# Optimization experiments

Measured on AMD Instinct MI355X. Metric: run time of the kernel, lower is better.

The kernel has to match this reference:

```python
import jax, jax.numpy as jnp
import numpy as np

B, H, S, D = 2, 16, 2048, 64  # batch, heads, seq (q_len=k_len), head dim (d_k=d_v)


def setup_inputs() -> dict:
    key = jax.random.key(0)
    kq, kk, kv = jax.random.split(key, 3)
    Q = jax.random.normal(kq, (B, H, S, D), dtype=jnp.float32)
    K = jax.random.normal(kk, (B, H, S, D), dtype=jnp.float32)
    V = jax.random.normal(kv, (B, H, S, D), dtype=jnp.float32)
    # causal 0/1 mask [q_len, k_len]; zeros get filled with -inf like masked_fill_
    mask = jnp.tril(jnp.ones((S, S), dtype=jnp.int32))
    return {"Q": Q, "K": K, "V": V, "mask": mask}


def reference(Q, K, V, mask):
    scale = K.shape[-1] ** 0.5
    # [B,H,q,k] = Q @ K^T / sqrt(d_k)
    scores = jnp.einsum("bhqd,bhkd->bhqk", Q, K) / scale
    # mask broadcast over batch/heads; mask==0 -> -inf
    scores = jnp.where(mask == 0, jnp.float32(-jnp.inf), scores)
    attn = jax.nn.softmax(scores, axis=-1)
    return jnp.einsum("bhqk,bhkd->bhqd", attn, V)
```

## Files before the change

kernel.cpp:

```cpp
#include <hip/hip_runtime.h>

#define S_LEN 2048
#define DHEAD 64
#define BK 64
#define NBH 32
#define QSCALE 0.18033688011112042f
#define THR 8.0f

typedef float f32x4 __attribute__((ext_vector_type(4)));
typedef __bf16 bf16x8 __attribute__((ext_vector_type(8)));
typedef unsigned short u16x8 __attribute__((ext_vector_type(8)));
typedef unsigned short u16x4 __attribute__((ext_vector_type(4)));
typedef unsigned int   u32x4 __attribute__((ext_vector_type(4)));
typedef unsigned int   u32x2 __attribute__((ext_vector_type(2)));

static __device__ __forceinline__ unsigned short bfr(float f) {
    return __builtin_bit_cast(unsigned short, (__bf16)f);
}
static __device__ __forceinline__ int swz(int row, int cb) {
    return row * 128 + (cb ^ ((row & 7) << 4));
}

#if __has_builtin(__builtin_amdgcn_permlane32_swap) && __has_builtin(__builtin_amdgcn_permlane16_swap)
#define HAVE_PLSWAP 1
static __device__ __forceinline__ void plswap32(unsigned& a, unsigned& b) {
    u32x2 r = __builtin_amdgcn_permlane32_swap(a, b, false, false);
    a = r[0]; b = r[1];
}
static __device__ __forceinline__ void plswap16(unsigned& a, unsigned& b) {
    u32x2 r = __builtin_amdgcn_permlane16_swap(a, b, false, false);
    a = r[0]; b = r[1];
}
static __device__ __forceinline__ float bcast_max4(float x) {
    unsigned a = __builtin_bit_cast(unsigned, x), b = a;
    plswap16(a, b);
    float m = fmaxf(__builtin_bit_cast(float, a), __builtin_bit_cast(float, b));
    unsigned c = __builtin_bit_cast(unsigned, m), d = c;
    plswap32(c, d);
    return fmaxf(__builtin_bit_cast(float, c), __builtin_bit_cast(float, d));
}
static __device__ __forceinline__ float bcast_sum4(float x) {
    unsigned a = __builtin_bit_cast(unsigned, x), b = a;
    plswap16(a, b);
    float s = __builtin_bit_cast(float, a) + __builtin_bit_cast(float, b);
    unsigned c = __builtin_bit_cast(unsigned, s), d = c;
    plswap32(c, d);
    return __builtin_bit_cast(float, c) + __builtin_bit_cast(float, d);
}
#else
#define HAVE_PLSWAP 0
static __device__ __forceinline__ void plswap32(unsigned& a, unsigned& b) {
    asm("v_permlane32_swap_b32 %0, %1" : "+v"(a), "+v"(b));
}
static __device__ __forceinline__ void plswap16(unsigned& a, unsigned& b) {
    asm("v_permlane16_swap_b32 %0, %1" : "+v"(a), "+v"(b));
}
static __device__ __forceinline__ float bcast_max4(float x) {
    x = fmaxf(x, __shfl_xor(x, 16));
    return fmaxf(x, __shfl_xor(x, 32));
}
static __device__ __forceinline__ float bcast_sum4(float x) {
    x += __shfl_xor(x, 16);
    return x + __shfl_xor(x, 32);
}
#endif

__global__ __launch_bounds__(256)
void cvt_bf16(const float* __restrict__ src, unsigned short* __restrict__ dst, int n4) {
    const int stride = gridDim.x * blockDim.x;
    for (int i = blockIdx.x * blockDim.x + threadIdx.x; i < n4; i += stride) {
        f32x4 v = ((const f32x4*)src)[i];
        u16x4 t;
        t[0] = bfr(v[0]); t[1] = bfr(v[1]); t[2] = bfr(v[2]); t[3] = bfr(v[3]);
        ((u16x4*)dst)[i] = t;
    }
}

__global__ __launch_bounds__(256)
void cvt_transpose_v(const float* __restrict__ V, unsigned short* __restrict__ Vt) {
    __shared__ unsigned short t2[64][72];
    const int bh = (int)blockIdx.x >> 5;
    const int st = (int)blockIdx.x & 31;
    const int t  = threadIdx.x;
    {
        const int sl = t >> 2, d0 = (t & 3) * 16;
        const float* src = V + ((size_t)bh * S_LEN + st * 64 + sl) * DHEAD + d0;
#pragma unroll
        for (int j = 0; j < 4; ++j) {
            f32x4 v = *(const f32x4*)(src + j * 4);
#pragma unroll
            for (int e = 0; e < 4; ++e) t2[sl][d0 + j * 4 + e] = bfr(v[e]);
        }
    }
    __syncthreads();
    const int d = t >> 2, sc = (t & 3) * 16;
    u16x8 a, b;
#pragma unroll
    for (int r = 0; r < 8; ++r) { a[r] = t2[sc + r][d]; b[r] = t2[sc + 8 + r][d]; }
    unsigned short* dst = Vt + ((size_t)bh * DHEAD + d) * S_LEN + st * 64 + sc;
    *(u16x8*)dst = a;
    *(u16x8*)(dst + 8) = b;
}

__global__ __launch_bounds__(256, 4)
void attn16r(const float* __restrict__ Qg,
             const unsigned short* __restrict__ Kb,
             const unsigned short* __restrict__ Vt,
             float* __restrict__ Og) {
    __shared__ __align__(16) unsigned short sK[2][BK * DHEAD];
    __shared__ __align__(16) unsigned short sV[2][DHEAD * BK];

    const int tid  = threadIdx.x;
    const int lane = tid & 63;
    const int w    = tid >> 6;
    const int idx = (int)blockIdx.x >> 5;
    const int bh  = (int)blockIdx.x & (NBH - 1);
    const int jj  = idx & 7, k4 = idx >> 3;
    const int blk_q = (k4 == 0) ? 31 - jj : (k4 == 1) ? jj
                    : (k4 == 2) ? 16 + jj : 15 - jj;
    const int q0 = blk_q * 64;
    const size_t base = (size_t)bh * (S_LEN * DHEAD);

    const int c = lane & 15;
    const int h = lane >> 4;

    const int srow = w * 8 + (lane >> 3);
    const int ch8  = ((lane & 7) ^ (lane >> 3)) * 8;
    const unsigned short* pK = Kb + base + (size_t)srow * DHEAD + ch8;
    const unsigned short* pV = Vt + base + (size_t)srow * S_LEN + ch8;

    auto issue = [&](int buf, int kt) {
        unsigned short* dK = &sK[buf][w * 512];
        unsigned short* dV = &sV[buf][w * 512];
        const unsigned short* gk = pK + (size_t)kt * 4096;
        const unsigned short* gv = pV + kt * 64;
#pragma unroll
        for (int i = 0; i < 2; ++i) {
            __builtin_amdgcn_global_load_lds(
                (const __attribute__((address_space(1))) unsigned int*)(gk + i * 2048),
                (__attribute__((address_space(3))) unsigned int*)(dK + i * 2048),
                16, 0, 0);
            __builtin_amdgcn_global_load_lds(
                (const __attribute__((address_space(1))) unsigned int*)(gv + (size_t)i * 32 * S_LEN),
                (__attribute__((address_space(3))) unsigned int*)(dV + i * 2048),
                16, 0, 0);
        }
    };

    bf16x8 qf[2];
    {
        const int qrow = q0 + w * 16 + c;
        const float* qp = Qg + base + (size_t)qrow * DHEAD + h * 8;
#pragma unroll
        for (int kk = 0; kk < 2; ++kk) {
            f32x4 a = *(const f32x4*)(qp + kk * 32);
            f32x4 b = *(const f32x4*)(qp + kk * 32 + 4);
            u16x8 t;
#pragma unroll
            for (int j = 0; j < 4; ++j) {
                t[j]     = bfr(a[j] * QSCALE);
                t[4 + j] = bfr(b[j] * QSCALE);
            }
            qf[kk] = __builtin_bit_cast(bf16x8, t);
        }
    }

    int offAB[4][2];
#pragma unroll
    for (int n = 0; n < 4; ++n)
#pragma unroll
        for (int kk = 0; kk < 2; ++kk)
            offAB[n][kk] = swz(n * 16 + c, (kk * 32 + h * 8) * 2);

    f32x4 o[4];
#pragma unroll
    for (int dn = 0; dn < 4; ++dn) o[dn] = (f32x4){0.f, 0.f, 0.f, 0.f};
    float m_run = -INFINITY, l_run = 0.f;

    issue(0, 0);
    int cur = 0;
    for (int kt = 0; kt <= blk_q; ++kt) {
        __syncthreads();
        if (kt < blk_q) issue(cur ^ 1, kt + 1);

        const char* sKc = (const char*)&sK[cur][0];
        const char* sVc = (const char*)&sV[cur][0];

        f32x4 st[4];
#pragma unroll
        for (int n = 0; n < 4; ++n) {
            f32x4 acc = (f32x4){0.f, 0.f, 0.f, 0.f};
#pragma unroll
            for (int kk = 0; kk < 2; ++kk) {
                u16x8 kf = *(const u16x8*)(sKc + offAB[n][kk]);
                acc = __builtin_amdgcn_mfma_f32_16x16x32_bf16(
                        __builtin_bit_cast(bf16x8, kf), qf[kk], acc, 0, 0, 0);
            }
            st[n] = acc;
        }

        bf16x8 vf[4][2];
#pragma unroll
        for (int dn = 0; dn < 4; ++dn)
#pragma unroll
            for (int kk = 0; kk < 2; ++kk)
                vf[dn][kk] = __builtin_bit_cast(bf16x8,
                                *(const u16x8*)(sVc + offAB[dn][kk]));

        if (kt == blk_q) {
            const int qg = q0 + w * 16 + c;
#pragma unroll
            for (int n = 0; n < 4; ++n)
#pragma unroll
                for (int r = 0; r < 4; ++r)
                    if (kt * BK + n * 16 + 4 * h + r > qg) st[n][r] = -INFINITY;
        }

        float mx = fmaxf(fmaxf(st[0][0], st[0][1]), fmaxf(st[0][2], st[0][3]));
#pragma unroll
        for (int n = 1; n < 4; ++n)
            mx = fmaxf(mx, fmaxf(fmaxf(st[n][0], st[n][1]), fmaxf(st[n][2], st[n][3])));
        mx = bcast_max4(mx);
        if (__any(mx > m_run + THR)) {
            const float mn = fmaxf(m_run, mx);
            const float al = exp2f(m_run - mn);
            m_run = mn;
            l_run *= al;
#pragma unroll
            for (int dn = 0; dn < 4; ++dn) o[dn] *= al;
        }
        float sum = 0.f;
#pragma unroll
        for (int n = 0; n < 4; ++n)
#pragma unroll
            for (int r = 0; r < 4; ++r) {
                float p = exp2f(st[n][r] - m_run);
                st[n][r] = p;
                sum += p;
            }
        l_run += sum;

        unsigned pd[4][2];
#pragma unroll
        for (int n = 0; n < 4; ++n) {
            pd[n][0] = (unsigned)bfr(st[n][0]) | ((unsigned)bfr(st[n][1]) << 16);
            pd[n][1] = (unsigned)bfr(st[n][2]) | ((unsigned)bfr(st[n][3]) << 16);
        }
        bf16x8 pb[2];
#pragma unroll
        for (int kk = 0; kk < 2; ++kk) {
            u32x4 fr;
#pragma unroll
            for (int X = 0; X < 2; ++X) {
                unsigned u = pd[2 * kk][X], v = pd[2 * kk + 1][X];
                plswap32(u, v);
                plswap16(u, v);
                fr[X]     = u;
                fr[2 + X] = v;
            }
            pb[kk] = __builtin_bit_cast(bf16x8, fr);
        }

#pragma unroll
        for (int dn = 0; dn < 4; ++dn)
#pragma unroll
            for (int kk = 0; kk < 2; ++kk)
                o[dn] = __builtin_amdgcn_mfma_f32_16x16x32_bf16(
                          vf[dn][kk], pb[kk], o[dn], 0, 0, 0);
        cur ^= 1;
    }

    const float inv = 1.0f / bcast_sum4(l_run);
    const int qg = q0 + w * 16 + c;
    float* op = Og + base + (size_t)qg * DHEAD + h * 4;
#pragma unroll
    for (int dn = 0; dn < 4; ++dn) {
        f32x4 t = o[dn] * inv;
        *(f32x4*)(op + dn * 16) = t;
    }
}

__global__ __launch_bounds__(256)
void attn_fb(const float* __restrict__ Qg, const float* __restrict__ K32,
             const float* __restrict__ V32, float* __restrict__ Og) {
    __shared__ __align__(16) unsigned short sK[2][BK * DHEAD];
    __shared__ __align__(16) unsigned short sV[2][DHEAD * BK];
    __shared__ __align__(16) unsigned short sP[4][16 * BK];

    const int tid  = threadIdx.x;
    const int lane = tid & 63;
    const int w    = tid >> 6;
    const int blk_q = 31 - ((int)blockIdx.x >> 5);
    const int bh    = (int)blockIdx.x & (NBH - 1);
    const int q0    = blk_q * 64;
    const size_t base = (size_t)bh * (S_LEN * DHEAD);

    const int col = lane & 15;
    const int hi  = lane >> 4;
    const int vkb = (tid >> 4) * 4;
    const int vdb = (tid & 15) * 4;
    const int fkr = tid >> 2;
    const int fkc = (tid & 3) * 16;

    f32x4 kr32[4], vr32[4];
    auto stage_issue = [&](int kt) {
        const float* kp = K32 + base + (size_t)(kt * BK + fkr) * DHEAD + fkc;
#pragma unroll
        for (int j = 0; j < 4; ++j) kr32[j] = *(const f32x4*)(kp + j * 4);
        const float* vp = V32 + base + (size_t)(kt * BK + vkb) * DHEAD + vdb;
#pragma unroll
        for (int j = 0; j < 4; ++j) vr32[j] = *(const f32x4*)(vp + j * DHEAD);
    };
    auto stage_write = [&](int buf) {
        char* sKb_ = (char*)&sK[buf][0];
        char* sVb_ = (char*)&sV[buf][0];
        u16x8 p0, p1;
#pragma unroll
        for (int j = 0; j < 4; ++j) {
            p0[j] = bfr(kr32[0][j]); p0[4 + j] = bfr(kr32[1][j]);
            p1[j] = bfr(kr32[2][j]); p1[4 + j] = bfr(kr32[3][j]);
        }
        *(u16x8*)(sKb_ + swz(fkr, fkc * 2))      = p0;
        *(u16x8*)(sKb_ + swz(fkr, fkc * 2 + 16)) = p1;
#pragma unroll
        for (int dd = 0; dd < 4; ++dd) {
            u16x4 t;
#pragma unroll
            for (int j = 0; j < 4; ++j) t[j] = bfr(vr32[j][dd]);
            *(u16x4*)(sVb_ + swz(vdb + dd, vkb * 2)) = t;
        }
    };

    bf16x8 qf[2];
    {
        const int qrow = q0 + w * 16 + col;
        const float* qp = Qg + base + (size_t)qrow * DHEAD + hi * 8;
#pragma unroll
        for (int kk = 0; kk < 2; ++kk) {
            f32x4 a = *(const f32x4*)(qp + kk * 32);
            f32x4 b = *(const f32x4*)(qp + kk * 32 + 4);
            u16x8 t;
#pragma unroll
            for (int j = 0; j < 4; ++j) {
                t[j]     = bfr(a[j] * QSCALE);
                t[4 + j] = bfr(b[j] * QSCALE);
            }
            qf[kk] = __builtin_bit_cast(bf16x8, t);
        }
    }

    int offAB[4][2];
#pragma unroll
    for (int n = 0; n < 4; ++n)
#pragma unroll
        for (int kk = 0; kk < 2; ++kk)
            offAB[n][kk] = swz(n * 16 + col, (kk * 32 + hi * 8) * 2);
    char* sPw = (char*)&sP[w][0];
    int offPS[4], offPL[2];
#pragma unroll
    for (int n = 0; n < 4; ++n)
        offPS[n] = col * 128 + ((n * 32 + hi * 8) ^ ((col & 7) << 4));
#pragma unroll
    for (int kk = 0; kk < 2; ++kk)
        offPL[kk] = col * 128 + ((kk * 64 + hi * 16) ^ ((col & 7) << 4));

    f32x4 o[4];
#pragma unroll
    for (int dn = 0; dn < 4; ++dn) o[dn] = (f32x4){0.f, 0.f, 0.f, 0.f};
    float m_run = -INFINITY, l_run = 0.f;

    stage_issue(0);
    stage_write(0);
    __syncthreads();

    int cur = 0;
    for (int kt = 0; kt <= blk_q; ++kt) {
        const char* sKc = (const char*)&sK[cur][0];
        const char* sVc = (const char*)&sV[cur][0];
        if (kt < blk_q) stage_issue(kt + 1);

        f32x4 st[4];
#pragma unroll
        for (int n = 0; n < 4; ++n) {
            f32x4 acc = (f32x4){0.f, 0.f, 0.f, 0.f};
#pragma unroll
            for (int kk = 0; kk < 2; ++kk) {
                u16x8 kf = *(const u16x8*)(sKc + offAB[n][kk]);
                acc = __builtin_amdgcn_mfma_f32_16x16x32_bf16(
                        __builtin_bit_cast(bf16x8, kf), qf[kk], acc, 0, 0, 0);
            }
            st[n] = acc;
        }
        if (kt == blk_q) {
            const int qg = q0 + w * 16 + col;
#pragma unroll
            for (int n = 0; n < 4; ++n)
#pragma unroll
                for (int r = 0; r < 4; ++r)
                    if (kt * BK + n * 16 + hi * 4 + r > qg) st[n][r] = -INFINITY;
        }
        float mx = fmaxf(fmaxf(st[0][0], st[0][1]), fmaxf(st[0][2], st[0][3]));
#pragma unroll
        for (int n = 1; n < 4; ++n)
            mx = fmaxf(mx, fmaxf(fmaxf(st[n][0], st[n][1]), fmaxf(st[n][2], st[n][3])));
        mx = fmaxf(mx, __shfl_xor(mx, 16));
        mx = fmaxf(mx, __shfl_xor(mx, 32));
        if (!__all(mx <= m_run + THR)) {
            const float mn = fmaxf(m_run, mx);
            const float al = exp2f(m_run - mn);
            m_run = mn;
            l_run *= al;
#pragma unroll
            for (int dn = 0; dn < 4; ++dn) o[dn] *= al;
        }
        float sum = 0.f;
#pragma unroll
        for (int n = 0; n < 4; ++n)
#pragma unroll
            for (int r = 0; r < 4; ++r) {
                float p = exp2f(st[n][r] - m_run);
                st[n][r] = p;
                sum += p;
            }
        sum += __shfl_xor(sum, 16);
        sum += __shfl_xor(sum, 32);
        l_run += sum;
#pragma unroll
        for (int n = 0; n < 4; ++n) {
            u16x4 t;
#pragma unroll
            for (int r = 0; r < 4; ++r) t[r] = bfr(st[n][r]);
            *(u16x4*)(sPw + offPS[n]) = t;
        }
        bf16x8 pb[2];
#pragma unroll
        for (int kk = 0; kk < 2; ++kk)
            pb[kk] = __builtin_bit_cast(bf16x8, *(const u16x8*)(sPw + offPL[kk]));
#pragma unroll
        for (int dn = 0; dn < 4; ++dn)
#pragma unroll
            for (int kk = 0; kk < 2; ++kk) {
                u16x8 vfr = *(const u16x8*)(sVc + offAB[dn][kk]);
                o[dn] = __builtin_amdgcn_mfma_f32_16x16x32_bf16(
                          __builtin_bit_cast(bf16x8, vfr), pb[kk], o[dn], 0, 0, 0);
            }
        if (kt < blk_q) stage_write(cur ^ 1);
        __syncthreads();
        cur ^= 1;
    }

    const float inv = 1.0f / l_run;
    const int qg = q0 + w * 16 + col;
    float* op = Og + base + (size_t)qg * DHEAD + hi * 4;
#pragma unroll
    for (int dn = 0; dn < 4; ++dn) {
        f32x4 t = o[dn] * inv;
        *(f32x4*)(op + dn * 16) = t;
    }
}

extern "C" void kernel_launch(void* const* d_in, const int* in_sizes, int n_in,
                              void* d_out, int out_size, void* d_ws, size_t ws_size,
                              hipStream_t stream) {
    const float* Q = (const float*)d_in[0];
    const float* K = (const float*)d_in[1];
    const float* V = (const float*)d_in[2];
    float* O = (float*)d_out;

    const size_t nelem = (size_t)NBH * S_LEN * DHEAD;
    const bool pre = ws_size >= 2 * nelem * sizeof(unsigned short);

    if (pre) {
        unsigned short* Kb = (unsigned short*)d_ws;
        unsigned short* Vt = Kb + nelem;
        cvt_bf16<<<2048, 256, 0, stream>>>(K, Kb, (int)(nelem / 4));
        cvt_transpose_v<<<NBH * (S_LEN / 64), 256, 0, stream>>>(V, Vt);
        attn16r<<<dim3(32 * NBH), 256, 0, stream>>>(Q, Kb, Vt, O);
    } else {
        attn_fb<<<dim3(32 * NBH), 256, 0, stream>>>(Q, K, V, O);
    }
}
```

Before: 58.18 us.

## Fold max subtraction into MFMA init, compute row sums via ones-MFMA

Initializes the QK^T MFMA accumulators with -m_run so scores arrive already shifted by the running max, removing a per-element subtraction. The lazy rescale test now compares against a fixed threshold and skips the cross-lane max broadcast on the common path. The softmax denominator is accumulated by an extra MFMA against a vector of ones, using the bf16-rounded P, which replaces scalar sums and the final cross-lane sum. s_setprio hints are added around the MFMA blocks. The trade-off is one more MFMA per k-step, and the running max starts at 0 rather than -inf.

Measured after the change: 57.45 us. No clear change (-1.3%).

```diff
diff --git a/kernel.cpp b/kernel.cpp
--- a/kernel.cpp
+++ b/kernel.cpp
@@ -22,7 +22,6 @@
 }
 
 #if __has_builtin(__builtin_amdgcn_permlane32_swap) && __has_builtin(__builtin_amdgcn_permlane16_swap)
-#define HAVE_PLSWAP 1
 static __device__ __forceinline__ void plswap32(unsigned& a, unsigned& b) {
     u32x2 r = __builtin_amdgcn_permlane32_swap(a, b, false, false);
     a = r[0]; b = r[1];
@@ -39,16 +38,7 @@
     plswap32(c, d);
     return fmaxf(__builtin_bit_cast(float, c), __builtin_bit_cast(float, d));
 }
-static __device__ __forceinline__ float bcast_sum4(float x) {
-    unsigned a = __builtin_bit_cast(unsigned, x), b = a;
-    plswap16(a, b);
-    float s = __builtin_bit_cast(float, a) + __builtin_bit_cast(float, b);
-    unsigned c = __builtin_bit_cast(unsigned, s), d = c;
-    plswap32(c, d);
-    return __builtin_bit_cast(float, c) + __builtin_bit_cast(float, d);
-}
 #else
-#define HAVE_PLSWAP 0
 static __device__ __forceinline__ void plswap32(unsigned& a, unsigned& b) {
     asm("v_permlane32_swap_b32 %0, %1" : "+v"(a), "+v"(b));
 }
@@ -58,10 +48,6 @@
 static __device__ __forceinline__ float bcast_max4(float x) {
     x = fmaxf(x, __shfl_xor(x, 16));
     return fmaxf(x, __shfl_xor(x, 32));
-}
-static __device__ __forceinline__ float bcast_sum4(float x) {
-    x += __shfl_xor(x, 16);
-    return x + __shfl_xor(x, 32);
 }
 #endif
 
@@ -165,6 +151,14 @@
         }
     }
 
+    bf16x8 onesf;
+    {
+        u16x8 t;
+#pragma unroll
+        for (int j = 0; j < 8; ++j) t[j] = 0x3F80;
+        onesf = __builtin_bit_cast(bf16x8, t);
+    }
+
     int offAB[4][2];
 #pragma unroll
     for (int n = 0; n < 4; ++n)
@@ -175,7 +169,8 @@
     f32x4 o[4];
 #pragma unroll
     for (int dn = 0; dn < 4; ++dn) o[dn] = (f32x4){0.f, 0.f, 0.f, 0.f};
-    float m_run = -INFINITY, l_run = 0.f;
+    f32x4 l4 = (f32x4){0.f, 0.f, 0.f, 0.f};
+    float m_run = 0.f;
 
     issue(0, 0);
     int cur = 0;
@@ -186,10 +181,12 @@
         const char* sKc = (const char*)&sK[cur][0];
         const char* sVc = (const char*)&sV[cur][0];
 
+        const float mb = -m_run;
         f32x4 st[4];
+        __builtin_amdgcn_s_setprio(1);
 #pragma unroll
         for (int n = 0; n < 4; ++n) {
-            f32x4 acc = (f32x4){0.f, 0.f, 0.f, 0.f};
+            f32x4 acc = (f32x4){mb, mb, mb, mb};
 #pragma unroll
             for (int kk = 0; kk < 2; ++kk) {
                 u16x8 kf = *(const u16x8*)(sKc + offAB[n][kk]);
@@ -198,6 +195,7 @@
             }
             st[n] = acc;
         }
+        __builtin_amdgcn_s_setprio(0);
 
         bf16x8 vf[4][2];
 #pragma unroll
@@ -216,29 +214,33 @@
                     if (kt * BK + n * 16 + 4 * h + r > qg) st[n][r] = -INFINITY;
         }
 
-        float mx = fmaxf(fmaxf(st[0][0], st[0][1]), fmaxf(st[0][2], st[0][3]));
-#pragma unroll
-        for (int n = 1; n < 4; ++n)
-            mx = fmaxf(mx, fmaxf(fmaxf(st[n][0], st[n][1]), fmaxf(st[n][2], st[n][3])));
-        mx = bcast_max4(mx);
-        if (__any(mx > m_run + THR)) {
-            const float mn = fmaxf(m_run, mx);
-            const float al = exp2f(m_run - mn);
-            m_run = mn;
-            l_run *= al;
+        const float a0 = fmaxf(fmaxf(st[0][0], st[0][1]), st[0][2]);
+        const float a1 = fmaxf(fmaxf(st[0][3], st[1][0]), st[1][1]);
+        const float a2 = fmaxf(fmaxf(st[1][2], st[1][3]), st[2][0]);
+        const float a3 = fmaxf(fmaxf(st[2][1], st[2][2]), st[2][3]);
+        const float a4 = fmaxf(fmaxf(st[3][0], st[3][1]), st[3][2]);
+        const float mx = fmaxf(fmaxf(fmaxf(a0, a1), fmaxf(a2, a3)),
+                               fmaxf(a4, st[3][3]));
+        if (__builtin_expect(__any(mx > THR), 0)) {
+            const float g  = bcast_max4(mx);
+            const float dl = fmaxf(g, 0.f);
+            const float al = exp2f(-dl);
+            m_run += dl;
+            l4 *= al;
 #pragma unroll
             for (int dn = 0; dn < 4; ++dn) o[dn] *= al;
-        }
-        float sum = 0.f;
-#pragma unroll
-        for (int n = 0; n < 4; ++n)
-#pragma unroll
-            for (int r = 0; r < 4; ++r) {
-                float p = exp2f(st[n][r] - m_run);
-                st[n][r] = p;
-                sum += p;
-            }
-        l_run += sum;
+#pragma unroll
+            for (int n = 0; n < 4; ++n)
+#pragma unroll
+                for (int r = 0; r < 4; ++r)
+                    st[n][r] = exp2f(st[n][r] - dl);
+        } else {
+#pragma unroll
+            for (int n = 0; n < 4; ++n)
+#pragma unroll
+                for (int r = 0; r < 4; ++r)
+                    st[n][r] = exp2f(st[n][r]);
+        }
 
         unsigned pd[4][2];
 #pragma unroll
@@ -261,16 +263,20 @@
             pb[kk] = __builtin_bit_cast(bf16x8, fr);
         }
 
-#pragma unroll
-        for (int dn = 0; dn < 4; ++dn)
-#pragma unroll
-            for (int kk = 0; kk < 2; ++kk)
+        __builtin_amdgcn_s_setprio(1);
+#pragma unroll
+        for (int kk = 0; kk < 2; ++kk) {
+            l4 = __builtin_amdgcn_mfma_f32_16x16x32_bf16(onesf, pb[kk], l4, 0, 0, 0);
+#pragma unroll
+            for (int dn = 0; dn < 4; ++dn)
                 o[dn] = __builtin_amdgcn_mfma_f32_16x16x32_bf16(
                           vf[dn][kk], pb[kk], o[dn], 0, 0, 0);
+        }
+        __builtin_amdgcn_s_setprio(0);
         cur ^= 1;
     }
 
-    const float inv = 1.0f / bcast_sum4(l_run);
+    const float inv = 1.0f / l4[0];
     const int qg = q0 + w * 16 + c;
     float* op = Og + base + (size_t)qg * DHEAD + h * 4;
 #pragma unroll
```
